# Kernel optimization log

Measured on AMD Instinct MI355X. Metric: run time of the kernel, lower is better.

The kernel has to match this reference:

```python
import jax, jax.numpy as jnp
import numpy as np

B, T, H, V = 256, 200, 256, 50000


def setup_inputs() -> dict:
    key = jax.random.key(0)
    ks = jax.random.split(key, 6)
    input_ids = jax.random.randint(ks[0], (B, T), 0, V, dtype=jnp.int64)
    lengths = jax.random.randint(ks[1], (B,), 1, T + 1, dtype=jnp.int32)
    scale = 1.0 / np.sqrt(H)
    emb = jax.random.normal(ks[2], (V + 1, H), dtype=jnp.float32) * 0.05
    w_ih = jax.random.normal(ks[3], (H, 3 * H), dtype=jnp.float32) * scale
    w_hh = jax.random.normal(ks[4], (H, 3 * H), dtype=jnp.float32) * scale
    b_ih = jnp.zeros((3 * H,), dtype=jnp.float32)
    b_hh = jnp.zeros((3 * H,), dtype=jnp.float32)
    return {"input_ids": input_ids, "lengths": lengths, "emb": emb,
            "w_ih": w_ih, "w_hh": w_hh, "b_ih": b_ih, "b_hh": b_hh}


def reference(input_ids, lengths, emb, w_ih, w_hh, b_ih, b_hh):
    # Embedding lookup: [B, T, H]
    x = emb[input_ids]
    # Precompute input-side gates for all timesteps: [B, T, 3H]
    gates_x = x @ w_ih + b_ih
    gates_x = jnp.moveaxis(gates_x, 1, 0)          # [T, B, 3H]
    t_idx = jnp.arange(T, dtype=lengths.dtype)
    mask = (t_idx[:, None] < lengths[None, :])[:, :, None]  # [T, B, 1]

    h0 = jnp.zeros((input_ids.shape[0], emb.shape[1]), dtype=emb.dtype)

    def step(h, inp):
        gx, m = inp
        rec = h @ w_hh + b_hh                       # [B, 3H] (reset_after=True)
        xz, xr, xh = jnp.split(gx, 3, axis=-1)
        rz, rr, rh = jnp.split(rec, 3, axis=-1)
        z = jax.nn.sigmoid(xz + rz)
        r = jax.nn.sigmoid(xr + rr)
        hh = jnp.tanh(xh + r * rh)
        h_new = z * h + (1.0 - z) * hh
        h = jnp.where(m, h_new, h)                  # skip padded timesteps
        return h, None

    h_final, _ = jax.lax.scan(step, h0, (gates_x, mask))
    logits = h_final @ emb.T                        # tied-embedding output: [B, V+1]
    return logits
```

## Files before the change

kernel.cpp:

```cpp
#include <hip/hip_runtime.h>
#include <hip/hip_fp16.h>

#define B_ 256
#define T_ 200
#define H_ 256
#define G3 768
#define NV 50001

typedef _Float16 half2v __attribute__((ext_vector_type(2)));
typedef _Float16 half4v __attribute__((ext_vector_type(4)));
typedef _Float16 half8v __attribute__((ext_vector_type(8)));
typedef float f32x4 __attribute__((ext_vector_type(4)));

union U32H2 { unsigned int u; half2v h; };

__device__ __forceinline__ float sigmoidf_(float x) {
  return 1.f / (1.f + __expf(-x));
}
__device__ __forceinline__ float tanhf_(float x) {
  float ax = fabsf(x);
  float e = __expf(-2.f * ax);
  float t = (1.f - e) / (1.f + e);
  return copysignf(t, x);
}
__device__ __forceinline__ f32x4 mfma16(half8v a, half8v b, f32x4 c) {
  return __builtin_amdgcn_mfma_f32_16x16x32_f16(a, b, c, 0, 0, 0);
}

__global__ __launch_bounds__(256) void pack_whh_frag(
    const float* __restrict__ whh, unsigned int* __restrict__ out) {
  int idx = blockIdx.x * 256 + threadIdx.x;
  int f = idx >> 8;
  int rem = idx & 255;
  int lane = rem >> 2;
  int jp = rem & 3;
  int nt = f >> 3, kc = f & 7;
  int col = nt * 16 + (lane & 15);
  int k = kc * 32 + (lane >> 4) * 8 + jp * 2;
  U32H2 u;
  u.h.x = (_Float16)whh[(size_t)k * G3 + col];
  u.h.y = (_Float16)whh[(size_t)(k + 1) * G3 + col];
  out[idx] = u.u;
}

__global__ __launch_bounds__(256) void pack_wiht(
    const float* __restrict__ wih, unsigned int* __restrict__ out) {
  int idx = blockIdx.x * 256 + threadIdx.x;
  int col = idx >> 7;
  int kk = (idx & 127) * 2;
  U32H2 u;
  u.h.x = (_Float16)wih[(size_t)kk * G3 + col];
  u.h.y = (_Float16)wih[(size_t)(kk + 1) * G3 + col];
  out[idx] = u.u;
}

__global__ __launch_bounds__(512) void gates_mfma(
    const int* __restrict__ ids, const float* __restrict__ emb,
    const __half* __restrict__ wih_t, const float* __restrict__ b_ih,
    __half* __restrict__ gates) {
  __shared__ __align__(16) _Float16 As[128 * 72];
  __shared__ __align__(16) _Float16 Bs[256 * 72];
  __shared__ int ids_s[128];
  __shared__ float bs[256];
  const int tid = threadIdx.x;
  const int r0 = blockIdx.x * 128;
  const int c0 = blockIdx.y * 256;
  const int w = tid >> 6, lane = tid & 63;
  const int wm = w >> 2, wn = w & 3;
  const int lr = lane & 15, lk = lane >> 4;

  if (tid < 128) ids_s[tid] = ids[r0 + tid];
  if (tid < 256) bs[tid] = b_ih[c0 + tid];
  __syncthreads();

  f32x4 acc[4][4];
#pragma unroll
  for (int i = 0; i < 4; ++i)
#pragma unroll
    for (int j = 0; j < 4; ++j) acc[i][j] = (f32x4){0.f, 0.f, 0.f, 0.f};

  for (int c = 0; c < 4; ++c) {
    const int kc = c * 64;
#pragma unroll
    for (int r4 = 0; r4 < 4; ++r4) {
      int q = tid + r4 * 512;
      int row = q >> 4;
      int kk = (q & 15) * 4;
      const float4 v = *(const float4*)&emb[(size_t)ids_s[row] * H_ + kc + kk];
      half4v hv = {(_Float16)v.x, (_Float16)v.y, (_Float16)v.z, (_Float16)v.w};
      *(half4v*)&As[row * 72 + kk] = hv;
    }
#pragma unroll
    for (int r4 = 0; r4 < 4; ++r4) {
      int q = tid + r4 * 512;
      int col = q >> 3;
      int cc = q & 7;
      uint4 v = *(const uint4*)((const unsigned short*)wih_t +
                                (size_t)(c0 + col) * H_ + kc + cc * 8);
      *(uint4*)&Bs[col * 72 + cc * 8] = v;
    }
    __syncthreads();
#pragma unroll
    for (int ks = 0; ks < 2; ++ks) {
      half8v af[4], bf[4];
#pragma unroll
      for (int i = 0; i < 4; ++i)
        af[i] = *(const half8v*)&As[(wm * 64 + i * 16 + lr) * 72 + ks * 32 + lk * 8];
#pragma unroll
      for (int j = 0; j < 4; ++j)
        bf[j] = *(const half8v*)&Bs[(wn * 64 + j * 16 + lr) * 72 + ks * 32 + lk * 8];
#pragma unroll
      for (int i = 0; i < 4; ++i)
#pragma unroll
        for (int j = 0; j < 4; ++j)
          acc[i][j] = mfma16(af[i], bf[j], acc[i][j]);
    }
    __syncthreads();
  }
#pragma unroll
  for (int j = 0; j < 4; ++j) {
    const int col = c0 + wn * 64 + j * 16 + lr;
    const float bj = bs[wn * 64 + j * 16 + lr];
#pragma unroll
    for (int i = 0; i < 4; ++i) {
      const int row = r0 + wm * 64 + i * 16 + lk * 4;
#pragma unroll
      for (int r = 0; r < 4; ++r)
        gates[(size_t)(row + r) * G3 + col] = (__half)(acc[i][j][r] + bj);
    }
  }
}

__global__ __launch_bounds__(512) void rec_m1(
    const int* __restrict__ lens, const unsigned int* __restrict__ whh_f,
    const float* __restrict__ b_hh, const __half* __restrict__ gates,
    float* __restrict__ hfin) {
  __shared__ __align__(16) uint4 Wl[144 * 64];
  __shared__ __align__(16) _Float16 hpk[256];
  const int tid = threadIdx.x;
  const int b = blockIdx.x;
  const int w = tid >> 6, lane = tid & 63;
  const int lr = lane & 15, lk = lane >> 4;

  const uint4* wf = (const uint4*)whh_f;

#pragma unroll
  for (int i = 0; i < 18; ++i) {
    int idx = tid + i * 512;
    int s = idx >> 6;
    int l = idx & 63;
    int nt = s / 3, kc = s - 3 * nt;
    Wl[s * 64 + l] = wf[(nt * 8 + kc) * 64 + l];
  }
  if (tid < 128) ((unsigned int*)hpk)[tid] = 0;

  int nt_[6];
#pragma unroll
  for (int p = 0; p < 6; ++p) nt_[p] = (p >> 1) * 16 + w * 2 + (p & 1);

  const int len = lens[b];
  float bhh[6];
  int gcol[6];
#pragma unroll
  for (int p = 0; p < 6; ++p) {
    int col = (p >> 1) * 256 + w * 32 + (p & 1) * 16 + lr;
    bhh[p] = b_hh[col];
    gcol[p] = col;
  }
  float h0 = 0.f, h1 = 0.f;
  __syncthreads();

  const __half* gb = gates + (size_t)b * T_ * G3;
  for (int t = 0; t < len; ++t) {
    float gx[6];
    if (lane < 16) {
      const __half* gt = gb + (size_t)t * G3;
#pragma unroll
      for (int p = 0; p < 6; ++p) gx[p] = (float)gt[gcol[p]];
    }
    uint4 sb[2][6];
#pragma unroll
    for (int p = 0; p < 6; ++p) sb[0][p] = wf[(nt_[p] * 8 + 3) * 64 + lane];
#pragma unroll
    for (int p = 0; p < 6; ++p) sb[1][p] = wf[(nt_[p] * 8 + 4) * 64 + lane];

    f32x4 acc[6];
#pragma unroll
    for (int p = 0; p < 6; ++p) acc[p] = (f32x4){0.f, 0.f, 0.f, 0.f};

#pragma unroll
    for (int kc = 0; kc < 3; ++kc) {
      half8v a = *(const half8v*)&hpk[kc * 32 + lk * 8];
#pragma unroll
      for (int p = 0; p < 6; ++p)
        acc[p] = mfma16(a, __builtin_bit_cast(half8v, Wl[(nt_[p] * 3 + kc) * 64 + lane]),
                        acc[p]);
    }
#pragma unroll
    for (int kc = 3; kc < 8; ++kc) {
      int bi = (kc - 3) & 1;
      half8v a = *(const half8v*)&hpk[kc * 32 + lk * 8];
#pragma unroll
      for (int p = 0; p < 6; ++p)
        acc[p] = mfma16(a, __builtin_bit_cast(half8v, sb[bi][p]), acc[p]);
      if (kc < 6) {
#pragma unroll
        for (int p = 0; p < 6; ++p)
          sb[bi][p] = wf[(nt_[p] * 8 + kc + 2) * 64 + lane];
      }
    }
    if (lane < 16) {
      float z0 = sigmoidf_(gx[0] + acc[0][0] + bhh[0]);
      float z1 = sigmoidf_(gx[1] + acc[1][0] + bhh[1]);
      float r0 = sigmoidf_(gx[2] + acc[2][0] + bhh[2]);
      float r1 = sigmoidf_(gx[3] + acc[3][0] + bhh[3]);
      float q0 = tanhf_(gx[4] + r0 * (acc[4][0] + bhh[4]));
      float q1 = tanhf_(gx[5] + r1 * (acc[5][0] + bhh[5]));
      h0 = z0 * h0 + (1.f - z0) * q0;
      h1 = z1 * h1 + (1.f - z1) * q1;
    }
    __syncthreads();
    if (lane < 16) {
      hpk[w * 32 + lr] = (_Float16)h0;
      hpk[w * 32 + 16 + lr] = (_Float16)h1;
    }
    __syncthreads();
  }
  if (lane < 16) {
    hfin[(size_t)b * H_ + w * 32 + lr] = h0;
    hfin[(size_t)b * H_ + w * 32 + 16 + lr] = h1;
  }
}

__global__ __launch_bounds__(512) void logits_mfma(
    const float* __restrict__ hfin, const float* __restrict__ emb,
    float* __restrict__ out) {
  __shared__ __align__(16) _Float16 As[256 * 72];
  __shared__ __align__(16) _Float16 Bs[64 * 72];
  const int tid = threadIdx.x;
  const int n0 = blockIdx.x * 64;
  const int w = tid >> 6, lane = tid & 63;
  const int wm = w >> 1, wn = w & 1;
  const int lr = lane & 15, lk = lane >> 4;

  f32x4 a1[4][2], a2[4][2];
#pragma unroll
  for (int i = 0; i < 4; ++i)
#pragma unroll
    for (int j = 0; j < 2; ++j) {
      a1[i][j] = (f32x4){0.f, 0.f, 0.f, 0.f};
      a2[i][j] = (f32x4){0.f, 0.f, 0.f, 0.f};
    }

  for (int c = 0; c < 8; ++c) {
    const int kc = c * 32;
#pragma unroll
    for (int r4 = 0; r4 < 4; ++r4) {
      int q = tid + r4 * 512;
      int row = q >> 3;
      int kk = (q & 7) * 4;
      float4 v = *(const float4*)&hfin[(size_t)row * H_ + kc + kk];
      half4v hi = {(_Float16)v.x, (_Float16)v.y, (_Float16)v.z, (_Float16)v.w};
      half4v lo = {(_Float16)((v.x - (float)hi.x) * 1024.f),
                   (_Float16)((v.y - (float)hi.y) * 1024.f),
                   (_Float16)((v.z - (float)hi.z) * 1024.f),
                   (_Float16)((v.w - (float)hi.w) * 1024.f)};
      int base = row * 72 + (kk >> 3) * 16 + (kk & 7);
      *(half4v*)&As[base] = hi;
      *(half4v*)&As[base + 8] = lo;
    }
    {
      int col = tid >> 3;
      int kk = (tid & 7) * 4;
      int n = n0 + col;
      float4 v = (n < NV) ? *(const float4*)&emb[(size_t)n * H_ + kc + kk]
                          : make_float4(0.f, 0.f, 0.f, 0.f);
      half4v hi = {(_Float16)v.x, (_Float16)v.y, (_Float16)v.z, (_Float16)v.w};
      half4v lo = {(_Float16)((v.x - (float)hi.x) * 1024.f),
                   (_Float16)((v.y - (float)hi.y) * 1024.f),
                   (_Float16)((v.z - (float)hi.z) * 1024.f),
                   (_Float16)((v.w - (float)hi.w) * 1024.f)};
      int base = col * 72 + (kk >> 3) * 16 + (kk & 7);
      *(half4v*)&Bs[base] = hi;
      *(half4v*)&Bs[base + 8] = lo;
    }
    __syncthreads();
    half8v ah[4], al[4];
#pragma unroll
    for (int i = 0; i < 4; ++i) {
      int base = (wm * 64 + i * 16 + lr) * 72 + lk * 16;
      ah[i] = *(const half8v*)&As[base];
      al[i] = *(const half8v*)&As[base + 8];
    }
#pragma unroll
    for (int j = 0; j < 2; ++j) {
      int base = (wn * 32 + j * 16 + lr) * 72 + lk * 16;
      half8v bh = *(const half8v*)&Bs[base];
      half8v bl = *(const half8v*)&Bs[base + 8];
#pragma unroll
      for (int i = 0; i < 4; ++i) {
        a1[i][j] = mfma16(ah[i], bh, a1[i][j]);
        a2[i][j] = mfma16(ah[i], bl, a2[i][j]);
        a2[i][j] = mfma16(al[i], bh, a2[i][j]);
      }
    }
    __syncthreads();
  }
#pragma unroll
  for (int j = 0; j < 2; ++j) {
    int n = n0 + wn * 32 + j * 16 + lr;
    if (n < NV) {
#pragma unroll
      for (int i = 0; i < 4; ++i) {
        int row = wm * 64 + i * 16 + lk * 4;
#pragma unroll
        for (int r = 0; r < 4; ++r)
          out[(size_t)(row + r) * NV + n] =
              a1[i][j][r] + a2[i][j][r] * (1.f / 1024.f);
      }
    }
  }
}

extern "C" void kernel_launch(void* const* d_in, const int* in_sizes, int n_in,
                              void* d_out, int out_size, void* d_ws, size_t ws_size,
                              hipStream_t stream) {
  const int* ids = (const int*)d_in[0];
  const int* lens = (const int*)d_in[1];
  const float* emb = (const float*)d_in[2];
  const float* w_ih = (const float*)d_in[3];
  const float* w_hh = (const float*)d_in[4];
  const float* b_ih = (const float*)d_in[5];
  const float* b_hh = (const float*)d_in[6];
  float* out = (float*)d_out;

  char* ws = (char*)d_ws;
  __half* gates = (__half*)ws;
  float* hfin = (float*)(ws + (size_t)B_ * T_ * G3 * sizeof(__half));
  unsigned int* whh_f =
      (unsigned int*)(ws + (size_t)B_ * T_ * G3 * sizeof(__half)
                      + (size_t)B_ * H_ * sizeof(float));
  unsigned int* wih_t = whh_f + (size_t)98304;

  pack_whh_frag<<<dim3(384), dim3(256), 0, stream>>>(w_hh, whh_f);
  pack_wiht<<<dim3(384), dim3(256), 0, stream>>>(w_ih, wih_t);
  gates_mfma<<<dim3(400, 3), dim3(512), 0, stream>>>(
      ids, emb, (const __half*)wih_t, b_ih, gates);
  rec_m1<<<dim3(B_), dim3(512), 0, stream>>>(lens, whh_f, b_hh, gates, hfin);
  logits_mfma<<<dim3((NV + 63) / 64), dim3(512), 0, stream>>>(hfin, emb, out);
}
```

Baseline: 505.3 us.

## Repack W_hh per wave, hold streamed weights in registers, double-buffer hidden state

W_hh is repacked so each wave's fragments sit contiguously, with the first three k-chunks in LDS and the rest streamed from global memory into 30 register slots. Those loads are issued through inline asm with manual vmcnt waits, so the next timestep's loads overlap the current MFMAs. The hidden state is double-buffered, which drops one of the two block barriers per step. The cost is hand-written waitcnt and asm that can break if the compiler reorders code, plus higher register pressure.

```diff
diff --git a/kernel.cpp b/kernel.cpp
--- a/kernel.cpp
+++ b/kernel.cpp
@@ -27,16 +27,19 @@
   return __builtin_amdgcn_mfma_f32_16x16x32_f16(a, b, c, 0, 0, 0);
 }
 
-__global__ __launch_bounds__(256) void pack_whh_frag(
+__global__ __launch_bounds__(256) void pack_whh_wv(
     const float* __restrict__ whh, unsigned int* __restrict__ out) {
   int idx = blockIdx.x * 256 + threadIdx.x;
-  int f = idx >> 8;
-  int rem = idx & 255;
-  int lane = rem >> 2;
-  int jp = rem & 3;
-  int nt = f >> 3, kc = f & 7;
-  int col = nt * 16 + (lane & 15);
-  int k = kc * 32 + (lane >> 4) * 8 + jp * 2;
+  int jp = idx & 3;
+  int l = (idx >> 2) & 63;
+  int rest = idx >> 8;
+  int p = rest % 6;
+  int rest2 = rest / 6;
+  int kc = rest2 & 7;
+  int w = rest2 >> 3;
+  int nt = (p >> 1) * 16 + w * 2 + (p & 1);
+  int col = nt * 16 + (l & 15);
+  int k = kc * 32 + (l >> 4) * 8 + jp * 2;
   U32H2 u;
   u.h.x = (_Float16)whh[(size_t)k * G3 + col];
   u.h.y = (_Float16)whh[(size_t)(k + 1) * G3 + col];
@@ -132,31 +135,36 @@
 }
 
 __global__ __launch_bounds__(512) void rec_m1(
-    const int* __restrict__ lens, const unsigned int* __restrict__ whh_f,
+    const int* __restrict__ lens, const unsigned int* __restrict__ whh_w,
     const float* __restrict__ b_hh, const __half* __restrict__ gates,
     float* __restrict__ hfin) {
-  __shared__ __align__(16) uint4 Wl[144 * 64];
-  __shared__ __align__(16) _Float16 hpk[256];
+  __shared__ __align__(16) uint4 Wl[8 * 18 * 64];
+  __shared__ __align__(16) _Float16 hpk[2][256];
   const int tid = threadIdx.x;
   const int b = blockIdx.x;
   const int w = tid >> 6, lane = tid & 63;
   const int lr = lane & 15, lk = lane >> 4;
 
-  const uint4* wf = (const uint4*)whh_f;
+  const uint4* wf = (const uint4*)whh_w;
+  const uint4* wfw = wf + (size_t)w * (48 * 64) + lane;
+
+  uint4 S3[6], S4[6], S5[6], S6[6], S7[6];
+#define LOADS(S, KC)                                                     \
+  _Pragma("unroll") for (int p = 0; p < 6; ++p) {                        \
+    asm volatile("global_load_dwordx4 %0, %1, off"                       \
+                 : "=v"(S[p])                                            \
+                 : "v"(wfw + (KC * 6 + p) * 64));                        \
+  }
+  LOADS(S3, 3) LOADS(S4, 4) LOADS(S5, 5) LOADS(S6, 6) LOADS(S7, 7)
 
 #pragma unroll
   for (int i = 0; i < 18; ++i) {
-    int idx = tid + i * 512;
-    int s = idx >> 6;
-    int l = idx & 63;
-    int nt = s / 3, kc = s - 3 * nt;
-    Wl[s * 64 + l] = wf[(nt * 8 + kc) * 64 + l];
-  }
-  if (tid < 128) ((unsigned int*)hpk)[tid] = 0;
-
-  int nt_[6];
-#pragma unroll
-  for (int p = 0; p < 6; ++p) nt_[p] = (p >> 1) * 16 + w * 2 + (p & 1);
+    int d = tid + i * 512;
+    int wv = d / 1152;
+    int r = d - wv * 1152;
+    Wl[d] = wf[(size_t)wv * (48 * 64) + r];
+  }
+  if (tid < 256) ((unsigned int*)hpk)[tid] = 0;
 
   const int len = lens[b];
   float bhh[6];
@@ -170,45 +178,46 @@
   float h0 = 0.f, h1 = 0.f;
   __syncthreads();
 
+  const uint4* WlW = Wl + w * 1152;
   const __half* gb = gates + (size_t)b * T_ * G3;
+
   for (int t = 0; t < len; ++t) {
+    const _Float16* hp = hpk[t & 1];
     float gx[6];
     if (lane < 16) {
       const __half* gt = gb + (size_t)t * G3;
 #pragma unroll
       for (int p = 0; p < 6; ++p) gx[p] = (float)gt[gcol[p]];
     }
-    uint4 sb[2][6];
-#pragma unroll
-    for (int p = 0; p < 6; ++p) sb[0][p] = wf[(nt_[p] * 8 + 3) * 64 + lane];
-#pragma unroll
-    for (int p = 0; p < 6; ++p) sb[1][p] = wf[(nt_[p] * 8 + 4) * 64 + lane];
-
     f32x4 acc[6];
 #pragma unroll
     for (int p = 0; p < 6; ++p) acc[p] = (f32x4){0.f, 0.f, 0.f, 0.f};
 
 #pragma unroll
     for (int kc = 0; kc < 3; ++kc) {
-      half8v a = *(const half8v*)&hpk[kc * 32 + lk * 8];
+      half8v a = *(const half8v*)&hp[kc * 32 + lk * 8];
 #pragma unroll
       for (int p = 0; p < 6; ++p)
-        acc[p] = mfma16(a, __builtin_bit_cast(half8v, Wl[(nt_[p] * 3 + kc) * 64 + lane]),
-                        acc[p]);
-    }
-#pragma unroll
-    for (int kc = 3; kc < 8; ++kc) {
-      int bi = (kc - 3) & 1;
-      half8v a = *(const half8v*)&hpk[kc * 32 + lk * 8];
-#pragma unroll
-      for (int p = 0; p < 6; ++p)
-        acc[p] = mfma16(a, __builtin_bit_cast(half8v, sb[bi][p]), acc[p]);
-      if (kc < 6) {
-#pragma unroll
-        for (int p = 0; p < 6; ++p)
-          sb[bi][p] = wf[(nt_[p] * 8 + kc + 2) * 64 + lane];
-      }
-    }
+        acc[p] = mfma16(
+            a, __builtin_bit_cast(half8v, WlW[(kc * 6 + p) * 64 + lane]),
+            acc[p]);
+    }
+#define PHASE(S, KC)                                                     \
+    {                                                                    \
+      asm volatile("s_waitcnt vmcnt(30)");                               \
+      __builtin_amdgcn_sched_barrier(0);                                 \
+      half8v a = *(const half8v*)&hp[KC * 32 + lk * 8];                  \
+      _Pragma("unroll") for (int p = 0; p < 6; ++p)                      \
+          acc[p] = mfma16(a, __builtin_bit_cast(half8v, S[p]), acc[p]);  \
+      _Pragma("unroll") for (int p = 0; p < 6; ++p) {                    \
+        asm volatile("global_load_dwordx4 %0, %1, off"                   \
+                     : "=v"(S[p])                                        \
+                     : "v"(wfw + (KC * 6 + p) * 64));                    \
+      }                                                                  \
+    }
+    PHASE(S3, 3) PHASE(S4, 4) PHASE(S5, 5) PHASE(S6, 6) PHASE(S7, 7)
+#undef PHASE
+
     if (lane < 16) {
       float z0 = sigmoidf_(gx[0] + acc[0][0] + bhh[0]);
       float z1 = sigmoidf_(gx[1] + acc[1][0] + bhh[1]);
@@ -218,14 +227,17 @@
       float q1 = tanhf_(gx[5] + r1 * (acc[5][0] + bhh[5]));
       h0 = z0 * h0 + (1.f - z0) * q0;
       h1 = z1 * h1 + (1.f - z1) * q1;
-    }
-    __syncthreads();
-    if (lane < 16) {
-      hpk[w * 32 + lr] = (_Float16)h0;
-      hpk[w * 32 + 16 + lr] = (_Float16)h1;
-    }
-    __syncthreads();
-  }
+      _Float16* hn = hpk[(t + 1) & 1];
+      hn[w * 32 + lr] = (_Float16)h0;
+      hn[w * 32 + 16 + lr] = (_Float16)h1;
+    }
+    __builtin_amdgcn_sched_barrier(0);
+    asm volatile("s_waitcnt lgkmcnt(0)");
+    __builtin_amdgcn_sched_barrier(0);
+    __builtin_amdgcn_s_barrier();
+    __builtin_amdgcn_sched_barrier(0);
+  }
+  asm volatile("s_waitcnt vmcnt(0)");
   if (lane < 16) {
     hfin[(size_t)b * H_ + w * 32 + lr] = h0;
     hfin[(size_t)b * H_ + w * 32 + 16 + lr] = h1;
@@ -337,15 +349,15 @@
   char* ws = (char*)d_ws;
   __half* gates = (__half*)ws;
   float* hfin = (float*)(ws + (size_t)B_ * T_ * G3 * sizeof(__half));
-  unsigned int* whh_f =
+  unsigned int* whh_w =
       (unsigned int*)(ws + (size_t)B_ * T_ * G3 * sizeof(__half)
                       + (size_t)B_ * H_ * sizeof(float));
-  unsigned int* wih_t = whh_f + (size_t)98304;
-
-  pack_whh_frag<<<dim3(384), dim3(256), 0, stream>>>(w_hh, whh_f);
+  unsigned int* wih_t = whh_w + (size_t)98304;
+
+  pack_whh_wv<<<dim3(384), dim3(256), 0, stream>>>(w_hh, whh_w);
   pack_wiht<<<dim3(384), dim3(256), 0, stream>>>(w_ih, wih_t);
   gates_mfma<<<dim3(400, 3), dim3(512), 0, stream>>>(
       ids, emb, (const __half*)wih_t, b_ih, gates);
-  rec_m1<<<dim3(B_), dim3(512), 0, stream>>>(lens, whh_f, b_hh, gates, hfin);
+  rec_m1<<<dim3(B_), dim3(512), 0, stream>>>(lens, whh_w, b_hh, gates, hfin);
   logits_mfma<<<dim3((NV + 63) / 64), dim3(512), 0, stream>>>(hfin, emb, out);
 }
```

Measured after the change: 717.3 us. +42.0%, slower.
